# Optimization experiments

Hardware: AMD Instinct MI355X
Metric: run time of the kernel (lower is better)

Reference implementation:

```python
import jax, jax.numpy as jnp
import numpy as np

NUM_CLASSES = 10
TEMPERATURE = 10.0
EPS = 1e-8


def _centers_counts(feat, label):
    # segment mean per class; counts used for validity masks
    counts = jax.ops.segment_sum(jnp.ones((feat.shape[0],), feat.dtype), label, NUM_CLASSES)
    sums = jax.ops.segment_sum(feat, label, NUM_CLASSES)
    centers = sums / jnp.maximum(counts, 1.0)[:, None]
    return centers, counts


def setup_inputs() -> dict:
    key = jax.random.key(0)
    k1, k2, k3, k4 = jax.random.split(key, 4)
    N, D = 262144, 64
    return {
        "feat1": jax.random.normal(k1, (N, D), dtype=jnp.float32),
        "label1": jax.random.randint(k2, (N,), 0, NUM_CLASSES, dtype=jnp.int32),
        "feat2": jax.random.normal(k3, (N, D), dtype=jnp.float32),
        "label2": jax.random.randint(k4, (N,), 0, NUM_CLASSES, dtype=jnp.int32),
    }


def reference(feat1, label1, feat2, label2):
    centers1, counts1 = _centers_counts(feat1, label1)   # [C, D], [C]
    centers2, counts2 = _centers_counts(feat2, label2)

    # per-sample euclidean distance to own class center
    d1 = jnp.sqrt(jnp.sum((feat1 - centers1[label1]) ** 2, axis=1))  # [N1]
    d2 = jnp.sqrt(jnp.sum((feat2 - centers2[label2]) ** 2, axis=1))  # [N2]

    # per-class mean distances (segment mean)
    m1 = jax.ops.segment_sum(d1, label1, NUM_CLASSES) / jnp.maximum(counts1, 1.0)
    m2 = jax.ops.segment_sum(d2, label2, NUM_CLASSES) / jnp.maximum(counts2, 1.0)

    # intra: only classes (present in label1, as torch.unique(label1)) with >1 members in both
    valid_intra = (counts1 > 1.0) & (counts2 > 1.0)
    intra_dist = jnp.sum(jnp.where(valid_intra, m1 + m2, 0.0))

    # inter: centers for classes present in both domains; mean over all pairwise distances
    valid_c = (counts1 > 0.0) & (counts2 > 0.0)  # [C]
    diff = centers1[:, None, :] - centers2[None, :, :]  # [C, C, D]
    pd = jnp.sqrt(jnp.sum(diff ** 2, axis=-1))           # [C, C]
    w = (valid_c[:, None] & valid_c[None, :]).astype(pd.dtype)
    n_valid = jnp.sum(valid_c.astype(pd.dtype))
    inter_dist = jnp.where(
        n_valid > 1.0,
        jnp.sum(pd * w) / jnp.maximum(n_valid * n_valid, 1.0),
        0.0,
    )

    normalized = intra_dist / (inter_dist + EPS)
    loss = jnp.where(
        inter_dist > 0.0,
        jnp.log1p(jnp.exp(normalized / TEMPERATURE)),
        intra_dist,
    )
    return loss
```

## Files before the change

### kernel.cpp

```cpp
#include <hip/hip_runtime.h>
#include <math.h>

#define NUM_CLASSES 10
#define D 64
#define NPART 8

#define PART_FLOATS 1320
#define OFF_SUMS1 0
#define OFF_SUMS2 640
#define OFF_CNT1  1280
#define OFF_CNT2  1290
#define OFF_DSUM1 1300
#define OFF_DSUM2 1310

__global__ __launch_bounds__(256) void k_pass1(
        const float* __restrict__ f1, const int* __restrict__ l1,
        const float* __restrict__ f2, const int* __restrict__ l2,
        int N, float* __restrict__ ws) {
    const float* f; const int* l; int base_s, base_c;
    if (blockIdx.y == 0) { f = f1; l = l1; base_s = OFF_SUMS1; base_c = OFF_CNT1; }
    else                 { f = f2; l = l2; base_s = OFF_SUMS2; base_c = OFF_CNT2; }
    float* wpart = ws + (size_t)(blockIdx.x & (NPART - 1)) * PART_FLOATS;

    __shared__ float bs[4][NUM_CLASSES][D];
    __shared__ float cshare[4][16];
    const int wv   = threadIdx.x >> 6;
    const int lane = threadIdx.x & 63;

    float acc[NUM_CLASSES];
#pragma unroll
    for (int c = 0; c < NUM_CLASSES; ++c) acc[c] = 0.0f;
    float vcnt = 0.0f;

    const int wid   = blockIdx.x * 4 + wv;
    const int nwave = gridDim.x * 4;

    for (int r0 = wid * 64; r0 < N; r0 += nwave * 64) {
        int r0u = __builtin_amdgcn_readfirstlane(r0);
        if (r0u + 64 <= N) {
#pragma unroll
            for (int q = 0; q < 4; ++q) {
                int lq[16];
                float v[16];
#pragma unroll
                for (int k = 0; k < 16; ++k)
                    lq[k] = l[r0u + q * 16 + k];
#pragma unroll
                for (int k = 0; k < 16; ++k)
                    v[k] = f[(size_t)(r0u + q * 16 + k) * D + lane];
#pragma unroll
                for (int k = 0; k < 16; ++k) {
                    int vlab;
                    asm("v_mov_b32 %0, %1" : "=v"(vlab) : "s"(lq[k]));
                    unsigned msk = 1u << vlab;
#pragma unroll
                    for (int c = 0; c < NUM_CLASSES; ++c)
                        acc[c] = fmaf((float)((msk >> c) & 1u), v[k], acc[c]);
                    vcnt += (float)((msk >> (lane & 15)) & 1u) *
                            ((lane < 16) ? 1.0f : 0.0f);
                }
            }
        } else {
            for (int rr = 0; rr < 64; ++rr) {
                int r = r0 + rr;
                if (r >= N) break;
                int lab = l[r];
                int vlab;
                asm("v_mov_b32 %0, %1" : "=v"(vlab) : "s"(lab));
                unsigned msk = 1u << vlab;
                float v = f[(size_t)r * D + lane];
#pragma unroll
                for (int c = 0; c < NUM_CLASSES; ++c)
                    acc[c] = fmaf((float)((msk >> c) & 1u), v, acc[c]);
                vcnt += (float)((msk >> (lane & 15)) & 1u) *
                        ((lane < 16) ? 1.0f : 0.0f);
            }
        }
    }

#pragma unroll
    for (int c = 0; c < NUM_CLASSES; ++c) bs[wv][c][lane] = acc[c];
    if (lane < 16) cshare[wv][lane] = vcnt;
    __syncthreads();

    for (int i = threadIdx.x; i < NUM_CLASSES * D; i += blockDim.x) {
        int cls = i >> 6, el = i & 63;
        float s = bs[0][cls][el] + bs[1][cls][el] + bs[2][cls][el] + bs[3][cls][el];
        atomicAdd(&wpart[base_s + i], s);
    }
    if (threadIdx.x < NUM_CLASSES) {
        float s = cshare[0][threadIdx.x] + cshare[1][threadIdx.x]
                + cshare[2][threadIdx.x] + cshare[3][threadIdx.x];
        atomicAdd(&wpart[base_c + threadIdx.x], s);
    }
}

__global__ void k_pass2(const float* __restrict__ f1, const int* __restrict__ l1,
                        const float* __restrict__ f2, const int* __restrict__ l2,
                        int N, float* __restrict__ ws) {
    const float* f; const int* l; int base_s, base_c, base_d;
    if (blockIdx.y == 0) { f = f1; l = l1; base_s = OFF_SUMS1; base_c = OFF_CNT1; base_d = OFF_DSUM1; }
    else                 { f = f2; l = l2; base_s = OFF_SUMS2; base_c = OFF_CNT2; base_d = OFF_DSUM2; }
    float* wpart = ws + (size_t)(blockIdx.x & (NPART - 1)) * PART_FLOATS;

    __shared__ float4 ctr[NUM_CLASSES * 17];
    __shared__ float  lcnt[NUM_CLASSES];
    __shared__ float  ld[NUM_CLASSES];
    float* ctrf = reinterpret_cast<float*>(ctr);

    if (threadIdx.x < NUM_CLASSES) {
        float s = 0.f;
#pragma unroll
        for (int p = 0; p < NPART; ++p)
            s += ws[p * PART_FLOATS + base_c + threadIdx.x];
        lcnt[threadIdx.x] = fmaxf(s, 1.0f);
        ld[threadIdx.x] = 0.f;
    }
    __syncthreads();
    for (int i = threadIdx.x; i < NUM_CLASSES * D; i += blockDim.x) {
        float a0 = ws[0 * PART_FLOATS + base_s + i];
        float a1 = ws[1 * PART_FLOATS + base_s + i];
        float a2 = ws[2 * PART_FLOATS + base_s + i];
        float a3 = ws[3 * PART_FLOATS + base_s + i];
        float a4 = ws[4 * PART_FLOATS + base_s + i];
        float a5 = ws[5 * PART_FLOATS + base_s + i];
        float a6 = ws[6 * PART_FLOATS + base_s + i];
        float a7 = ws[7 * PART_FLOATS + base_s + i];
        float s = ((a0 + a1) + (a2 + a3)) + ((a4 + a5) + (a6 + a7));
        ctrf[(i >> 6) * 68 + (i & 63)] = s / lcnt[i >> 6];
    }
    __syncthreads();

    const int j = threadIdx.x & 3;
    int g       = blockIdx.x * (blockDim.x >> 2) + (threadIdx.x >> 2);
    const int G = gridDim.x * (blockDim.x >> 2);
    const float4* f4 = reinterpret_cast<const float4*>(f);

    for (int row = g; row < N; row += G) {
        int lab = l[row];
        size_t rb = (size_t)row * 16;
        float4 v0 = f4[rb + 0 + j];
        float4 v1 = f4[rb + 4 + j];
        float4 v2 = f4[rb + 8 + j];
        float4 v3 = f4[rb + 12 + j];
        const float4* cc = &ctr[lab * 17];
        float4 c0 = cc[0 + j], c1 = cc[4 + j], c2 = cc[8 + j], c3 = cc[12 + j];
        float s = 0.f, x;
        x = v0.x - c0.x; s = fmaf(x, x, s); x = v0.y - c0.y; s = fmaf(x, x, s);
        x = v0.z - c0.z; s = fmaf(x, x, s); x = v0.w - c0.w; s = fmaf(x, x, s);
        x = v1.x - c1.x; s = fmaf(x, x, s); x = v1.y - c1.y; s = fmaf(x, x, s);
        x = v1.z - c1.z; s = fmaf(x, x, s); x = v1.w - c1.w; s = fmaf(x, x, s);
        x = v2.x - c2.x; s = fmaf(x, x, s); x = v2.y - c2.y; s = fmaf(x, x, s);
        x = v2.z - c2.z; s = fmaf(x, x, s); x = v2.w - c2.w; s = fmaf(x, x, s);
        x = v3.x - c3.x; s = fmaf(x, x, s); x = v3.y - c3.y; s = fmaf(x, x, s);
        x = v3.z - c3.z; s = fmaf(x, x, s); x = v3.w - c3.w; s = fmaf(x, x, s);
        s += __shfl_xor(s, 1);
        s += __shfl_xor(s, 2);
        if (j == 0) atomicAdd(&ld[lab], sqrtf(s));
    }
    __syncthreads();
    if (threadIdx.x < NUM_CLASSES)
        atomicAdd(&wpart[base_d + threadIdx.x], ld[threadIdx.x]);
}

__global__ void k_final(const float* __restrict__ ws, float* __restrict__ out) {
    __shared__ float c1[NUM_CLASSES * D];
    __shared__ float c2[NUM_CLASSES * D];
    __shared__ float cnt1[NUM_CLASSES], cnt2[NUM_CLASSES], ds1[NUM_CLASSES], ds2[NUM_CLASSES];
    __shared__ float pd[NUM_CLASSES * NUM_CLASSES];

    if (threadIdx.x < 4 * NUM_CLASSES) {
        int which = threadIdx.x / NUM_CLASSES, c = threadIdx.x % NUM_CLASSES;
        int off = (which == 0 ? OFF_CNT1 : which == 1 ? OFF_CNT2
                 : which == 2 ? OFF_DSUM1 : OFF_DSUM2) + c;
        float s = 0.f;
#pragma unroll
        for (int p = 0; p < NPART; ++p) s += ws[p * PART_FLOATS + off];
        (which == 0 ? cnt1 : which == 1 ? cnt2 : which == 2 ? ds1 : ds2)[c] = s;
    }
    __syncthreads();
    for (int i = threadIdx.x; i < NUM_CLASSES * D; i += blockDim.x) {
        float a = 0.f, b = 0.f;
#pragma unroll
        for (int p = 0; p < NPART; ++p) {
            a += ws[p * PART_FLOATS + OFF_SUMS1 + i];
            b += ws[p * PART_FLOATS + OFF_SUMS2 + i];
        }
        int cls = i >> 6;
        c1[i] = a / fmaxf(cnt1[cls], 1.0f);
        c2[i] = b / fmaxf(cnt2[cls], 1.0f);
    }
    __syncthreads();

    if (threadIdx.x < NUM_CLASSES * NUM_CLASSES) {
        int i = threadIdx.x / NUM_CLASSES;
        int j = threadIdx.x % NUM_CLASSES;
        float s = 0.f;
        for (int d = 0; d < D; ++d) {
            float df = c1[i * D + d] - c2[j * D + d];
            s += df * df;
        }
        pd[threadIdx.x] = sqrtf(s);
    }
    __syncthreads();

    if (threadIdx.x == 0) {
        float intra = 0.f;
        for (int c = 0; c < NUM_CLASSES; ++c) {
            if (cnt1[c] > 1.0f && cnt2[c] > 1.0f) {
                float m1 = ds1[c] / fmaxf(cnt1[c], 1.0f);
                float m2 = ds2[c] / fmaxf(cnt2[c], 1.0f);
                intra += m1 + m2;
            }
        }
        float n_valid = 0.f;
        for (int i = 0; i < NUM_CLASSES; ++i)
            if (cnt1[i] > 0.0f && cnt2[i] > 0.0f) n_valid += 1.0f;
        float inter_sum = 0.f;
        for (int i = 0; i < NUM_CLASSES; ++i) {
            bool vi = cnt1[i] > 0.0f && cnt2[i] > 0.0f;
            for (int j = 0; j < NUM_CLASSES; ++j) {
                bool vj = cnt1[j] > 0.0f && cnt2[j] > 0.0f;
                if (vi && vj) inter_sum += pd[i * NUM_CLASSES + j];
            }
        }
        float inter = (n_valid > 1.0f) ? inter_sum / fmaxf(n_valid * n_valid, 1.0f) : 0.0f;
        float normalized = intra / (inter + 1e-8f);
        float x = normalized / 10.0f;
        float softplus = (x > 0.0f) ? (x + log1pf(expf(-x))) : log1pf(expf(x));
        float loss = (inter > 0.0f) ? softplus : intra;
        out[0] = loss;
    }
}

extern "C" void kernel_launch(void* const* d_in, const int* in_sizes, int n_in,
                              void* d_out, int out_size, void* d_ws, size_t ws_size,
                              hipStream_t stream) {
    const float* f1 = (const float*)d_in[0];
    const int*   l1 = (const int*)d_in[1];
    const float* f2 = (const float*)d_in[2];
    const int*   l2 = (const int*)d_in[3];
    float* ws  = (float*)d_ws;
    float* out = (float*)d_out;
    const int N = in_sizes[1];

    hipMemsetAsync(d_ws, 0, (size_t)NPART * PART_FLOATS * sizeof(float), stream);
    dim3 grid1(512, 2);
    k_pass1<<<grid1, 256, 0, stream>>>(f1, l1, f2, l2, N, ws);
    dim3 grid2(1024, 2);
    k_pass2<<<grid2, 256, 0, stream>>>(f1, l1, f2, l2, N, ws);
    k_final<<<1, 128, 0, stream>>>(ws, out);
}
```

Before: 77.57 us.

## Vectorize pass1 with float4 row-slot loads, packed labels, and shuffle reduction

Pass 1 now has each lane load a float4 covering a quarter row, so a wavefront handles four rows per load instead of one. Labels are packed into 4-bit fields so each slot can pull out its own row's label. The per-lane class accumulators become float4 and are reduced across the four row slots with xor shuffles before going to shared memory. The grid for pass 1 is also doubled. The aim is fewer, wider memory instructions and less per-row scalar overhead, at the cost of more accumulator registers and extra shuffle work at the end.

```diff
diff --git a/kernel.cpp b/kernel.cpp
--- a/kernel.cpp
+++ b/kernel.cpp
@@ -24,40 +24,50 @@
 
     __shared__ float bs[4][NUM_CLASSES][D];
     __shared__ float cshare[4][16];
-    const int wv   = threadIdx.x >> 6;
-    const int lane = threadIdx.x & 63;
-
-    float acc[NUM_CLASSES];
-#pragma unroll
-    for (int c = 0; c < NUM_CLASSES; ++c) acc[c] = 0.0f;
+    const int wv    = threadIdx.x >> 6;
+    const int lane  = threadIdx.x & 63;
+    const int chunk = lane & 15;
+    const int slot  = lane >> 4;
+    const int sh    = slot * 4;
+
+    float4 acc[NUM_CLASSES];
+#pragma unroll
+    for (int c = 0; c < NUM_CLASSES; ++c) acc[c] = make_float4(0.f, 0.f, 0.f, 0.f);
     float vcnt = 0.0f;
 
     const int wid   = blockIdx.x * 4 + wv;
     const int nwave = gridDim.x * 4;
+    const float4* f4p = reinterpret_cast<const float4*>(f);
 
     for (int r0 = wid * 64; r0 < N; r0 += nwave * 64) {
         int r0u = __builtin_amdgcn_readfirstlane(r0);
         if (r0u + 64 <= N) {
 #pragma unroll
-            for (int q = 0; q < 4; ++q) {
-                int lq[16];
-                float v[16];
-#pragma unroll
-                for (int k = 0; k < 16; ++k)
-                    lq[k] = l[r0u + q * 16 + k];
-#pragma unroll
-                for (int k = 0; k < 16; ++k)
-                    v[k] = f[(size_t)(r0u + q * 16 + k) * D + lane];
-#pragma unroll
-                for (int k = 0; k < 16; ++k) {
-                    int vlab;
-                    asm("v_mov_b32 %0, %1" : "=v"(vlab) : "s"(lq[k]));
-                    unsigned msk = 1u << vlab;
-#pragma unroll
-                    for (int c = 0; c < NUM_CLASSES; ++c)
-                        acc[c] = fmaf((float)((msk >> c) & 1u), v[k], acc[c]);
-                    vcnt += (float)((msk >> (lane & 15)) & 1u) *
-                            ((lane < 16) ? 1.0f : 0.0f);
+            for (int b = 0; b < 4; ++b) {
+                const int rb = r0u + b * 16;
+                float4 v0 = f4p[(size_t)(rb + 0 + slot) * 16 + chunk];
+                float4 v1 = f4p[(size_t)(rb + 4 + slot) * 16 + chunk];
+                float4 v2 = f4p[(size_t)(rb + 8 + slot) * 16 + chunk];
+                float4 v3 = f4p[(size_t)(rb + 12 + slot) * 16 + chunk];
+                int p0 = l[rb + 0] | (l[rb + 1] << 4) | (l[rb + 2] << 8) | (l[rb + 3] << 12);
+                int p1 = l[rb + 4] | (l[rb + 5] << 4) | (l[rb + 6] << 8) | (l[rb + 7] << 12);
+                int p2 = l[rb + 8] | (l[rb + 9] << 4) | (l[rb + 10] << 8) | (l[rb + 11] << 12);
+                int p3 = l[rb + 12] | (l[rb + 13] << 4) | (l[rb + 14] << 8) | (l[rb + 15] << 12);
+#pragma unroll
+                for (int g = 0; g < 4; ++g) {
+                    int packed = (g == 0) ? p0 : (g == 1) ? p1 : (g == 2) ? p2 : p3;
+                    float4 v   = (g == 0) ? v0 : (g == 1) ? v1 : (g == 2) ? v2 : v3;
+                    int lab = (packed >> sh) & 15;
+                    unsigned msk = 1u << lab;
+#pragma unroll
+                    for (int c = 0; c < NUM_CLASSES; ++c) {
+                        float m = (float)((msk >> c) & 1u);
+                        acc[c].x = fmaf(m, v.x, acc[c].x);
+                        acc[c].y = fmaf(m, v.y, acc[c].y);
+                        acc[c].z = fmaf(m, v.z, acc[c].z);
+                        acc[c].w = fmaf(m, v.w, acc[c].w);
+                    }
+                    vcnt += (float)((msk >> chunk) & 1u);
                 }
             }
         } else {
@@ -65,22 +75,43 @@
                 int r = r0 + rr;
                 if (r >= N) break;
                 int lab = l[r];
-                int vlab;
-                asm("v_mov_b32 %0, %1" : "=v"(vlab) : "s"(lab));
-                unsigned msk = 1u << vlab;
-                float v = f[(size_t)r * D + lane];
-#pragma unroll
-                for (int c = 0; c < NUM_CLASSES; ++c)
-                    acc[c] = fmaf((float)((msk >> c) & 1u), v, acc[c]);
-                vcnt += (float)((msk >> (lane & 15)) & 1u) *
-                        ((lane < 16) ? 1.0f : 0.0f);
-            }
-        }
-    }
-
-#pragma unroll
-    for (int c = 0; c < NUM_CLASSES; ++c) bs[wv][c][lane] = acc[c];
-    if (lane < 16) cshare[wv][lane] = vcnt;
+                float4 v = f4p[(size_t)r * 16 + chunk];
+                unsigned msk = 1u << lab;
+                if (slot == 0) {
+#pragma unroll
+                    for (int c = 0; c < NUM_CLASSES; ++c) {
+                        float m = (float)((msk >> c) & 1u);
+                        acc[c].x = fmaf(m, v.x, acc[c].x);
+                        acc[c].y = fmaf(m, v.y, acc[c].y);
+                        acc[c].z = fmaf(m, v.z, acc[c].z);
+                        acc[c].w = fmaf(m, v.w, acc[c].w);
+                    }
+                    vcnt += (float)((msk >> chunk) & 1u);
+                }
+            }
+        }
+    }
+
+#pragma unroll
+    for (int c = 0; c < NUM_CLASSES; ++c) {
+#pragma unroll
+        for (int s = 16; s < 64; s <<= 1) {
+            acc[c].x += __shfl_xor(acc[c].x, s);
+            acc[c].y += __shfl_xor(acc[c].y, s);
+            acc[c].z += __shfl_xor(acc[c].z, s);
+            acc[c].w += __shfl_xor(acc[c].w, s);
+        }
+    }
+    vcnt += __shfl_xor(vcnt, 16);
+    vcnt += __shfl_xor(vcnt, 32);
+
+    if (lane < 16) {
+        float4* bsf4 = reinterpret_cast<float4*>(&bs[wv][0][0]);
+#pragma unroll
+        for (int c = 0; c < NUM_CLASSES; ++c)
+            bsf4[c * 16 + chunk] = acc[c];
+        cshare[wv][chunk] = vcnt;
+    }
     __syncthreads();
 
     for (int i = threadIdx.x; i < NUM_CLASSES * D; i += blockDim.x) {
@@ -245,7 +276,7 @@
     const int N = in_sizes[1];
 
     hipMemsetAsync(d_ws, 0, (size_t)NPART * PART_FLOATS * sizeof(float), stream);
-    dim3 grid1(512, 2);
+    dim3 grid1(1024, 2);
     k_pass1<<<grid1, 256, 0, stream>>>(f1, l1, f2, l2, N, ws);
     dim3 grid2(1024, 2);
     k_pass2<<<grid2, 256, 0, stream>>>(f1, l1, f2, l2, N, ws);
```

After: 73.81 us, median of 2. 1.05x faster.
